# Kernel tuning notes

Measured on AMD Instinct MI355X. Metric: run time of the kernel, lower is better.

The kernel has to match this reference:

```python
import jax, jax.numpy as jnp
import numpy as np

NN_SIZE = 16  # nn_size from __init__


def _knn_idx(points_ref, k):
    """Brute-force KNN of points_ref against itself (replaces faiss_knn).
    Returns (B, N, k) neighbor indices, self point excluded."""
    sq = jnp.sum(points_ref * points_ref, axis=-1)  # (B, N)
    # squared pairwise distances (B, N, N)
    d2 = sq[:, :, None] + sq[:, None, :] - 2.0 * jnp.einsum(
        'bnd,bmd->bnm', points_ref, points_ref)
    _, idx = jax.lax.top_k(-d2, k + 1)  # nearest first; idx[...,0] is self
    return idx[:, :, 1:]


def _edge_lengths(pts, knn_idx):
    """Gather neighbor coords and compute edge lengths (B, N, K)."""
    group = jax.vmap(lambda p, i: p[i])(pts, knn_idx)  # (B, N, K, D)
    return jnp.linalg.norm(group - pts[:, :, None, :], axis=-1)


def setup_inputs() -> dict:
    key = jax.random.key(0)
    k1, k2 = jax.random.split(key)
    B, N, D = 4, 8192, 3
    points_ref = jax.random.normal(k1, (B, N, D), dtype=jnp.float32)
    # pred points: perturbed ref so the loss is non-degenerate
    points = points_ref + 0.01 * jax.random.normal(k2, (B, N, D), dtype=jnp.float32)
    return {"points_ref": points_ref, "points": points}


def reference(points_ref, points):
    # faiss KNN is non-differentiable -> stop_gradient on the index search
    knn_idx = _knn_idx(jax.lax.stop_gradient(points_ref), NN_SIZE)  # (B,N,K)
    dist_ref = _edge_lengths(points_ref, knn_idx)  # (B, N, K)
    dist = _edge_lengths(points, knn_idx)          # (B, N, K)
    # metric = torch.nn.L1Loss() (mean reduction)
    return jnp.mean(jnp.abs(dist_ref - dist))
```

## Files before the change

### kernel.cpp

```cpp
#include <hip/hip_runtime.h>
#include <math.h>

#define BATCH 4
#define NPTS  8192
#define KNN   16
#define KK    17
#define NQ    (BATCH*NPTS)
#define JMASK 0x1FFFu
#define EMASK 0xFFFFE000u
#define TOTAL_EDGES (BATCH*NPTS*KNN)

#define GC    32
#define GLO   (-4.5f)
#define GINV  (32.0f/9.0f)
#define NCELL (GC*GC*GC)

#define NG    128
#define GSZ   64

#define QPB   16
#define BLOCK 256
#define GRIDQ (NQ/QPB)
#define WIN   64
#define CAP   21

__device__ __forceinline__ int cell_coord(float x) {
    int c = (int)floorf((x - GLO) * GINV);
    return min(GC - 1, max(0, c));
}
__device__ __forceinline__ unsigned spread5(unsigned v) {
    v &= 31u;
    v = (v | (v << 8)) & 0x100Fu;
    v = (v | (v << 4)) & 0x10C3u;
    v = (v | (v << 2)) & 0x1249u;
    return v;
}
__device__ __forceinline__ unsigned morton_id(float x, float y, float z) {
    return spread5((unsigned)cell_coord(x)) | (spread5((unsigned)cell_coord(y)) << 1)
         | (spread5((unsigned)cell_coord(z)) << 2);
}
__device__ __forceinline__ unsigned mkkey(const float4 p, float xi, float yi,
                                          float zi, float sqi, unsigned j) {
    const float e  = fmaf(p.x, xi, fmaf(p.y, yi, p.z * zi)) + p.w;
    const float d2 = e + sqi;
    return (__float_as_uint(d2) & EMASK) | j;
}
__device__ __forceinline__ void ins17(unsigned (&a)[KK], unsigned key) {
    #pragma unroll
    for (int k = KK - 1; k >= 1; --k) a[k] = min(a[k], max(a[k - 1], key));
    a[0] = min(a[0], key);
}
template<int RL>
__device__ __forceinline__ unsigned merge_tau(const unsigned (*s_key)[BLOCK], int t) {
    const int mq = t & (QPB - 1), half = (t >> 4) & 1;
    unsigned m[KK];
    #pragma unroll
    for (int k = 0; k < KK; ++k) m[k] = 0xFFFFFFFFu;
    for (int s = 8 * half; s < 8 * half + 8; ++s) {
        const int col = mq + s * QPB;
        for (int k = 0; k < RL; ++k) {
            const unsigned c = s_key[k][col];
            if (c >= m[KK - 1]) break;
            ins17(m, c);
        }
    }
    unsigned tau = 0;
    #pragma unroll
    for (int k = 0; k < KK; ++k) {
        const unsigned bk = (unsigned)__shfl_xor((int)m[KK - 1 - k], 16, 64);
        tau = max(tau, min(m[k], bk));
    }
    return tau;
}

__global__ void pel_hist(const float* __restrict__ pref, unsigned* __restrict__ hist,
                         float* __restrict__ acc, unsigned* __restrict__ bcnt) {
    const int idx = blockIdx.x * 256 + threadIdx.x;
    if (idx == 0) { acc[0] = 0.0f; bcnt[0] = 0u; }
    const int b = idx >> 13;
    const unsigned mid = morton_id(pref[3*idx], pref[3*idx+1], pref[3*idx+2]);
    atomicAdd(&hist[b * NCELL + mid], 1u);
}
__global__ __launch_bounds__(1024)
void pel_scan(const unsigned* __restrict__ hist, unsigned* __restrict__ off) {
    __shared__ unsigned s[1024];
    const unsigned* h = hist + blockIdx.x * NCELL;
    unsigned*       o = off  + blockIdx.x * NCELL;
    const int t = threadIdx.x;
    unsigned v[32], tot = 0;
    #pragma unroll
    for (int k = 0; k < 32; ++k) { v[k] = h[t * 32 + k]; tot += v[k]; }
    s[t] = tot;
    __syncthreads();
    for (int d = 1; d < 1024; d <<= 1) {
        const unsigned add = (t >= d) ? s[t - d] : 0u;
        __syncthreads();
        s[t] += add;
        __syncthreads();
    }
    unsigned run = s[t] - tot;
    #pragma unroll
    for (int k = 0; k < 32; ++k) { o[t * 32 + k] = run; run += v[k]; }
}
__global__ void pel_scatter(const float* __restrict__ pref, const float* __restrict__ pts,
                            unsigned* __restrict__ off,
                            float4* __restrict__ p4r, float4* __restrict__ p4p) {
    const int idx = blockIdx.x * 256 + threadIdx.x;
    const int b = idx >> 13;
    const float x = pref[3*idx], y = pref[3*idx+1], z = pref[3*idx+2];
    const unsigned mid = morton_id(x, y, z);
    const unsigned pos = atomicAdd(&off[b * NCELL + mid], 1u);
    p4r[b * NPTS + pos] = make_float4(-2.f*x, -2.f*y, -2.f*z, fmaf(x, x, fmaf(y, y, z*z)));
    const float px = pts[3*idx], py = pts[3*idx+1], pz = pts[3*idx+2];
    p4p[b * NPTS + pos] = make_float4(-2.f*px, -2.f*py, -2.f*pz,
                                      fmaf(px, px, fmaf(py, py, pz*pz)));
}
__global__ __launch_bounds__(256)
void pel_gstat(const float4* __restrict__ P4r, float4* __restrict__ gball) {
    const int wv = threadIdx.x >> 6, lane = threadIdx.x & 63;
    const int gid = blockIdx.x * 4 + wv;
    const int b = gid >> 7, g = gid & (NG - 1);
    const float4 p = P4r[b * NPTS + g * GSZ + lane];
    const float x = -0.5f * p.x, y = -0.5f * p.y, z = -0.5f * p.z;
    float mnx = x, mxx = x, mny = y, mxy = y, mnz = z, mxz = z;
    #pragma unroll
    for (int m = 1; m <= 32; m <<= 1) {
        mnx = fminf(mnx, __shfl_xor(mnx, m, 64)); mxx = fmaxf(mxx, __shfl_xor(mxx, m, 64));
        mny = fminf(mny, __shfl_xor(mny, m, 64)); mxy = fmaxf(mxy, __shfl_xor(mxy, m, 64));
        mnz = fminf(mnz, __shfl_xor(mnz, m, 64)); mxz = fmaxf(mxz, __shfl_xor(mxz, m, 64));
    }
    const float cx = 0.5f * (mnx + mxx), cy = 0.5f * (mny + mxy), cz = 0.5f * (mnz + mxz);
    float d = sqrtf((x-cx)*(x-cx) + (y-cy)*(y-cy) + (z-cz)*(z-cz));
    #pragma unroll
    for (int m = 1; m <= 32; m <<= 1) d = fmaxf(d, __shfl_xor(d, m, 64));
    if (lane == 0) gball[gid] = make_float4(cx, cy, cz, d);
}

__global__ __launch_bounds__(BLOCK, 8)
void pel_query(const float4* __restrict__ P4r, const float4* __restrict__ P4p,
               const float4* __restrict__ gball,
               float* __restrict__ acc_ws, unsigned* __restrict__ bcnt,
               float* __restrict__ out)
{
    __shared__ unsigned s_key[CAP][BLOCK];
    __shared__ unsigned s_tau[QPB];
    __shared__ unsigned short s_glist[NG];
    __shared__ float s_grp[4];
    __shared__ int s_ng;
    __shared__ float s_part[BLOCK / 64];

    const int t  = threadIdx.x;
    const int lq = t & (QPB - 1), sp = t >> 4;
    const int q  = blockIdx.x * QPB + lq;
    const int b  = q >> 13;
    const int i  = q & (NPTS - 1);

    const float4* __restrict__ Pq = P4r + b * NPTS;
    const float4* __restrict__ Pp = P4p + b * NPTS;
    const float4* __restrict__ Gb = gball + b * NG;

    const float4 self = Pq[i];
    const float xi = -0.5f * self.x, yi = -0.5f * self.y, zi = -0.5f * self.z;
    const float sqi = self.w;

    unsigned al[4] = {~0u, ~0u, ~0u, ~0u};
    const int w0 = min(max(i - WIN / 2, 0), NPTS - WIN) + sp * 4;
    {
        float4 cw[4];
        #pragma unroll
        for (int u = 0; u < 4; ++u) cw[u] = Pq[w0 + u];
        #pragma unroll
        for (int u = 0; u < 4; ++u) {
            const unsigned key = mkkey(cw[u], xi, yi, zi, sqi, (unsigned)(w0 + u));
            #pragma unroll
            for (int k = 3; k >= 1; --k) al[k] = min(al[k], max(al[k - 1], key));
            al[0] = min(al[0], key);
        }
    }
    #pragma unroll
    for (int k = 0; k < 4; ++k) s_key[k][t] = al[k];
    __syncthreads();
    if (t < 32) {
        const unsigned tau0 = merge_tau<4>(s_key, t);
        if (t < QPB) s_tau[t] = tau0;
    }
    __syncthreads();

    if (t < QPB) {
        if (t == 0) s_ng = 0;
        const int i2 = (blockIdx.x * QPB + t) & (NPTS - 1);
        const float4 s2 = Pq[i2];
        const float qx = -0.5f * s2.x, qy = -0.5f * s2.y, qz = -0.5f * s2.z;
        float mnx = qx, mxx = qx, mny = qy, mxy = qy, mnz = qz, mxz = qz;
        #pragma unroll
        for (int m = 1; m <= 8; m <<= 1) {
            mnx = fminf(mnx, __shfl_xor(mnx, m, 64)); mxx = fmaxf(mxx, __shfl_xor(mxx, m, 64));
            mny = fminf(mny, __shfl_xor(mny, m, 64)); mxy = fmaxf(mxy, __shfl_xor(mxy, m, 64));
            mnz = fminf(mnz, __shfl_xor(mnz, m, 64)); mxz = fmaxf(mxz, __shfl_xor(mxz, m, 64));
        }
        const float cx = 0.5f * (mnx + mxx), cy = 0.5f * (mny + mxy), cz = 0.5f * (mnz + mxz);
        const float dq = sqrtf((qx-cx)*(qx-cx) + (qy-cy)*(qy-cy) + (qz-cz)*(qz-cz));
        const float rt = sqrtf(__uint_as_float((s_tau[t] & EMASK) + 0x2000u));
        float v = dq + rt;
        #pragma unroll
        for (int m = 1; m <= 8; m <<= 1) v = fmaxf(v, __shfl_xor(v, m, 64));
        if (t == 0) {
            s_grp[0] = cx; s_grp[1] = cy; s_grp[2] = cz; s_grp[3] = v + 1e-3f;
        }
    }
    __syncthreads();

    if (t < NG) {
        const float4 gb = Gb[t];
        const float dx = gb.x - s_grp[0], dy = gb.y - s_grp[1], dz = gb.z - s_grp[2];
        const float rhs = s_grp[3] + gb.w;
        if (dx*dx + dy*dy + dz*dz <= rhs * rhs) {
            const int slot = atomicAdd(&s_ng, 1);
            s_glist[slot] = (unsigned short)t;
        }
    }
    __syncthreads();
    const int ng = s_ng;

    unsigned tauL = s_tau[lq];
    int cnt = 0;
    for (int gi = 0; gi < ng; ++gi) {
        const int gb4 = (int)s_glist[gi] * GSZ + sp * 4;
        float4 c[4];
        #pragma unroll
        for (int u = 0; u < 4; ++u) c[u] = Pq[gb4 + u];
        #pragma unroll
        for (int u = 0; u < 4; ++u) {
            const unsigned key = mkkey(c[u], xi, yi, zi, sqi, (unsigned)(gb4 + u));
            s_key[cnt][t] = key;
            cnt += (key <= tauL) ? 1 : 0;
        }
        if (cnt > CAP - 4) {
            unsigned k17[KK];
            #pragma unroll
            for (int k = 0; k < KK; ++k) k17[k] = 0xFFFFFFFFu;
            for (int n = 0; n < cnt; ++n) ins17(k17, s_key[n][t]);
            const unsigned th = k17[KK - 1];
            int kept = 0;
            for (int n = 0; n < cnt; ++n) {
                const unsigned c2 = s_key[n][t];
                if (c2 <= th) { s_key[kept][t] = c2; ++kept; }
            }
            cnt = kept; tauL = min(tauL, th);
        }
    }

    unsigned c17[KK];
    #pragma unroll
    for (int k = 0; k < KK; ++k) c17[k] = 0xFFFFFFFFu;
    for (int n = 0; n < cnt; ++n) ins17(c17, s_key[n][t]);
    __syncthreads();
    #pragma unroll
    for (int k = 0; k < KK; ++k) s_key[k][t] = c17[k];
    __syncthreads();
    if (t < 32) {
        const unsigned tauX = merge_tau<KK>(s_key, t);
        if (t < QPB) s_tau[t] = tauX;
    }
    __syncthreads();
    const unsigned tauK = s_tau[lq];

    const float4 selfp = Pp[i];
    const float pxi = -0.5f * selfp.x, pyi = -0.5f * selfp.y, pzi = -0.5f * selfp.z;
    float accv = 0.0f;
    #pragma unroll
    for (int k = 0; k < KK; ++k) {
        if (c17[k] <= tauK) {
            const int j = (int)(c17[k] & JMASK);
            const float4 pr = Pq[j];
            const float er  = fmaf(pr.x, xi, fmaf(pr.y, yi, pr.z * zi)) + pr.w;
            const float d2r = fmaxf(er + sqi, 0.0f);
            const float4 pp = Pp[j];
            const float ep  = fmaf(pp.x, pxi, fmaf(pp.y, pyi, pp.z * pzi)) + pp.w;
            const float d2p = fmaxf(ep + selfp.w, 0.0f);
            accv += fabsf(sqrtf(d2r) - sqrtf(d2p));
        }
    }

    #pragma unroll
    for (int o = 32; o > 0; o >>= 1) accv += __shfl_down(accv, o, 64);
    if ((t & 63) == 0) s_part[t >> 6] = accv;
    __syncthreads();
    if (t == 0) {
        float s = 0.0f;
        #pragma unroll
        for (int w2 = 0; w2 < BLOCK / 64; ++w2) s += s_part[w2];
        atomicAdd(acc_ws, s);
        __threadfence();
        const unsigned old = atomicAdd(bcnt, 1u);
        if (old == GRIDQ - 1) {
            __threadfence();
            const float total = atomicAdd(acc_ws, 0.0f);
            out[0] = total * (1.0f / (float)TOTAL_EDGES);
        }
    }
}

extern "C" void kernel_launch(void* const* d_in, const int* in_sizes, int n_in,
                              void* d_out, int out_size, void* d_ws, size_t ws_size,
                              hipStream_t stream) {
    const float* pref = (const float*)d_in[0];
    const float* pts  = (const float*)d_in[1];
    float4*   P4r  = (float4*)d_ws;
    float4*   P4p  = P4r + NQ;
    unsigned* hist = (unsigned*)d_ws;
    unsigned* off  = (unsigned*)((char*)d_ws + 1048576);
    float4*   gball= (float4*)((char*)d_ws + 1572864);
    float*    acc  = (float*)((char*)d_ws + 1581056);
    unsigned* bcnt = (unsigned*)(acc + 1);
    float*    out  = (float*)d_out;

    hipMemsetAsync(hist, 0, BATCH * NCELL * sizeof(unsigned), stream);
    pel_hist   <<<NQ / 256, 256, 0, stream>>>(pref, hist, acc, bcnt);
    pel_scan   <<<BATCH, 1024, 0, stream>>>(hist, off);
    pel_scatter<<<NQ / 256, 256, 0, stream>>>(pref, pts, off, P4r, P4p);
    pel_gstat  <<<(BATCH * NG) / 4, 256, 0, stream>>>(P4r, gball);
    pel_query  <<<GRIDQ, BLOCK, 0, stream>>>(P4r, P4p, gball, acc, bcnt, out);
}
```

Baseline: 254.9 us.

## Stage candidate groups in shared memory tiles and swizzle block order

Candidate points from up to 16 selected groups are now loaded cooperatively by the whole block into an LDS tile. Every thread then reads them from shared memory instead of issuing per-thread global float4 loads for each group. Block IDs are remapped so that consecutive blocks spread across query groups, and launch bounds drop from 8 to 4 blocks per CU to make room for the extra LDS. The cost is added __syncthreads per tile, more LDS use and possibly lower occupancy.

```diff
diff --git a/kernel.cpp b/kernel.cpp
--- a/kernel.cpp
+++ b/kernel.cpp
@@ -23,6 +23,7 @@
 #define GRIDQ (NQ/QPB)
 #define WIN   64
 #define CAP   21
+#define SG    16
 
 __device__ __forceinline__ int cell_coord(float x) {
     int c = (int)floorf((x - GLO) * GINV);
@@ -136,13 +137,15 @@
     if (lane == 0) gball[gid] = make_float4(cx, cy, cz, d);
 }
 
-__global__ __launch_bounds__(BLOCK, 8)
+__global__ __launch_bounds__(BLOCK, 4)
 void pel_query(const float4* __restrict__ P4r, const float4* __restrict__ P4p,
                const float4* __restrict__ gball,
                float* __restrict__ acc_ws, unsigned* __restrict__ bcnt,
                float* __restrict__ out)
 {
     __shared__ unsigned s_key[CAP][BLOCK];
+    __shared__ float4 s_cand[SG * GSZ];
+    __shared__ unsigned s_gbase[SG];
     __shared__ unsigned s_tau[QPB];
     __shared__ unsigned short s_glist[NG];
     __shared__ float s_grp[4];
@@ -151,7 +154,9 @@
 
     const int t  = threadIdx.x;
     const int lq = t & (QPB - 1), sp = t >> 4;
-    const int q  = blockIdx.x * QPB + lq;
+    const int bid = blockIdx.x;
+    const int qg  = ((bid & 7) << 8) | (bid >> 3);
+    const int q  = qg * QPB + lq;
     const int b  = q >> 13;
     const int i  = q & (NPTS - 1);
 
@@ -188,7 +193,7 @@
 
     if (t < QPB) {
         if (t == 0) s_ng = 0;
-        const int i2 = (blockIdx.x * QPB + t) & (NPTS - 1);
+        const int i2 = (qg * QPB + t) & (NPTS - 1);
         const float4 s2 = Pq[i2];
         const float qx = -0.5f * s2.x, qy = -0.5f * s2.y, qz = -0.5f * s2.z;
         float mnx = qx, mxx = qx, mny = qy, mxy = qy, mnz = qz, mxz = qz;
@@ -224,29 +229,48 @@
 
     unsigned tauL = s_tau[lq];
     int cnt = 0;
-    for (int gi = 0; gi < ng; ++gi) {
-        const int gb4 = (int)s_glist[gi] * GSZ + sp * 4;
-        float4 c[4];
-        #pragma unroll
-        for (int u = 0; u < 4; ++u) c[u] = Pq[gb4 + u];
-        #pragma unroll
-        for (int u = 0; u < 4; ++u) {
-            const unsigned key = mkkey(c[u], xi, yi, zi, sqi, (unsigned)(gb4 + u));
-            s_key[cnt][t] = key;
-            cnt += (key <= tauL) ? 1 : 0;
-        }
-        if (cnt > CAP - 4) {
-            unsigned k17[KK];
+    for (int tile = 0; tile < ng; tile += SG) {
+        const int tng = min(SG, ng - tile);
+        __syncthreads();
+        if (t < tng) s_gbase[t] = (unsigned)s_glist[tile + t] * GSZ;
+        {
+            unsigned srcs[4]; int mm[4]; int nm = 0;
+            for (int m = t; m < tng * GSZ; m += BLOCK) {
+                mm[nm] = m;
+                srcs[nm] = (unsigned)s_glist[tile + (m >> 6)] * GSZ + (m & 63);
+                ++nm;
+            }
+            float4 vals[4];
+            for (int k = 0; k < nm; ++k) vals[k] = Pq[srcs[k]];
+            for (int k = 0; k < nm; ++k) s_cand[mm[k]] = vals[k];
+        }
+        __syncthreads();
+        const int nsteps = tng * 4;
+        for (int mblk = 0; mblk < nsteps; mblk += 4) {
+            const unsigned jbase = s_gbase[mblk >> 2];
+            float4 c[4];
             #pragma unroll
-            for (int k = 0; k < KK; ++k) k17[k] = 0xFFFFFFFFu;
-            for (int n = 0; n < cnt; ++n) ins17(k17, s_key[n][t]);
-            const unsigned th = k17[KK - 1];
-            int kept = 0;
-            for (int n = 0; n < cnt; ++n) {
-                const unsigned c2 = s_key[n][t];
-                if (c2 <= th) { s_key[kept][t] = c2; ++kept; }
+            for (int u = 0; u < 4; ++u) c[u] = s_cand[(mblk + u) * 16 + sp];
+            #pragma unroll
+            for (int u = 0; u < 4; ++u) {
+                const unsigned j = jbase + (unsigned)(((mblk + u) * 16 + sp) & 63);
+                const unsigned key = mkkey(c[u], xi, yi, zi, sqi, j);
+                s_key[cnt][t] = key;
+                cnt += (key <= tauL) ? 1 : 0;
             }
-            cnt = kept; tauL = min(tauL, th);
+            if (cnt > CAP - 4) {
+                unsigned k17[KK];
+                #pragma unroll
+                for (int k = 0; k < KK; ++k) k17[k] = 0xFFFFFFFFu;
+                for (int n = 0; n < cnt; ++n) ins17(k17, s_key[n][t]);
+                const unsigned th = k17[KK - 1];
+                int kept = 0;
+                for (int n = 0; n < cnt; ++n) {
+                    const unsigned c2 = s_key[n][t];
+                    if (c2 <= th) { s_key[kept][t] = c2; ++kept; }
+                }
+                cnt = kept; tauL = min(tauL, th);
+            }
         }
     }
 
```

After: 351.5 us. 1.38x slower.

## Scan a contiguous group range, coarsen the Morton grid, and swizzle query blocks

Applied to the files above, without the earlier changes.

The query kernel now keeps only the minimum and maximum index of the overlapping point groups and scans that whole contiguous range, rather than building an explicit list of overlapping groups. Each thread takes a contiguous chunk of the range instead of 4 points per group. The Morton grid is coarsened from 32^3 to 16^3 cells, which shrinks the histogram and prefix-scan work, and block indices are swizzled to reorder queries across the grid. The range scan drops the shared-memory list but may visit many groups that do not overlap, and the coarser grid gives a looser spatial sort.

```diff
diff --git a/kernel.cpp b/kernel.cpp
--- a/kernel.cpp
+++ b/kernel.cpp
@@ -10,9 +10,9 @@
 #define EMASK 0xFFFFE000u
 #define TOTAL_EDGES (BATCH*NPTS*KNN)
 
-#define GC    32
+#define GC    16
 #define GLO   (-4.5f)
-#define GINV  (32.0f/9.0f)
+#define GINV  (16.0f/9.0f)
 #define NCELL (GC*GC*GC)
 
 #define NG    128
@@ -28,16 +28,15 @@
     int c = (int)floorf((x - GLO) * GINV);
     return min(GC - 1, max(0, c));
 }
-__device__ __forceinline__ unsigned spread5(unsigned v) {
-    v &= 31u;
-    v = (v | (v << 8)) & 0x100Fu;
-    v = (v | (v << 4)) & 0x10C3u;
-    v = (v | (v << 2)) & 0x1249u;
+__device__ __forceinline__ unsigned spread4(unsigned v) {
+    v &= 15u;
+    v = (v | (v << 4)) & 0xC3u;
+    v = (v | (v << 2)) & 0x249u;
     return v;
 }
 __device__ __forceinline__ unsigned morton_id(float x, float y, float z) {
-    return spread5((unsigned)cell_coord(x)) | (spread5((unsigned)cell_coord(y)) << 1)
-         | (spread5((unsigned)cell_coord(z)) << 2);
+    return spread4((unsigned)cell_coord(x)) | (spread4((unsigned)cell_coord(y)) << 1)
+         | (spread4((unsigned)cell_coord(z)) << 2);
 }
 __device__ __forceinline__ unsigned mkkey(const float4 p, float xi, float yi,
                                           float zi, float sqi, unsigned j) {
@@ -87,9 +86,9 @@
     const unsigned* h = hist + blockIdx.x * NCELL;
     unsigned*       o = off  + blockIdx.x * NCELL;
     const int t = threadIdx.x;
-    unsigned v[32], tot = 0;
-    #pragma unroll
-    for (int k = 0; k < 32; ++k) { v[k] = h[t * 32 + k]; tot += v[k]; }
+    unsigned v[4], tot = 0;
+    #pragma unroll
+    for (int k = 0; k < 4; ++k) { v[k] = h[t * 4 + k]; tot += v[k]; }
     s[t] = tot;
     __syncthreads();
     for (int d = 1; d < 1024; d <<= 1) {
@@ -100,7 +99,7 @@
     }
     unsigned run = s[t] - tot;
     #pragma unroll
-    for (int k = 0; k < 32; ++k) { o[t * 32 + k] = run; run += v[k]; }
+    for (int k = 0; k < 4; ++k) { o[t * 4 + k] = run; run += v[k]; }
 }
 __global__ void pel_scatter(const float* __restrict__ pref, const float* __restrict__ pts,
                             unsigned* __restrict__ off,
@@ -144,14 +143,15 @@
 {
     __shared__ unsigned s_key[CAP][BLOCK];
     __shared__ unsigned s_tau[QPB];
-    __shared__ unsigned short s_glist[NG];
     __shared__ float s_grp[4];
-    __shared__ int s_ng;
+    __shared__ int s_glo, s_ghi;
     __shared__ float s_part[BLOCK / 64];
 
     const int t  = threadIdx.x;
     const int lq = t & (QPB - 1), sp = t >> 4;
-    const int q  = blockIdx.x * QPB + lq;
+    const int bid = blockIdx.x;
+    const int qg  = ((bid & 7) << 8) | (bid >> 3);
+    const int q  = qg * QPB + lq;
     const int b  = q >> 13;
     const int i  = q & (NPTS - 1);
 
@@ -187,8 +187,8 @@
     __syncthreads();
 
     if (t < QPB) {
-        if (t == 0) s_ng = 0;
-        const int i2 = (blockIdx.x * QPB + t) & (NPTS - 1);
+        if (t == 0) { s_glo = NG; s_ghi = 0; }
+        const int i2 = (qg * QPB + t) & (NPTS - 1);
         const float4 s2 = Pq[i2];
         const float qx = -0.5f * s2.x, qy = -0.5f * s2.y, qz = -0.5f * s2.z;
         float mnx = qx, mxx = qx, mny = qy, mxy = qy, mnz = qz, mxz = qz;
@@ -215,23 +215,24 @@
         const float dx = gb.x - s_grp[0], dy = gb.y - s_grp[1], dz = gb.z - s_grp[2];
         const float rhs = s_grp[3] + gb.w;
         if (dx*dx + dy*dy + dz*dz <= rhs * rhs) {
-            const int slot = atomicAdd(&s_ng, 1);
-            s_glist[slot] = (unsigned short)t;
-        }
-    }
-    __syncthreads();
-    const int ng = s_ng;
+            atomicMin(&s_glo, t);
+            atomicMax(&s_ghi, t);
+        }
+    }
+    __syncthreads();
+    const int glo = s_glo, ghi = s_ghi;
 
     unsigned tauL = s_tau[lq];
     int cnt = 0;
-    for (int gi = 0; gi < ng; ++gi) {
-        const int gb4 = (int)s_glist[gi] * GSZ + sp * 4;
+    const int csz = (ghi - glo + 1) * 4;
+    const int c0  = glo * GSZ + sp * csz;
+    for (int j = c0; j < c0 + csz; j += 4) {
         float4 c[4];
         #pragma unroll
-        for (int u = 0; u < 4; ++u) c[u] = Pq[gb4 + u];
+        for (int u = 0; u < 4; ++u) c[u] = Pq[j + u];
         #pragma unroll
         for (int u = 0; u < 4; ++u) {
-            const unsigned key = mkkey(c[u], xi, yi, zi, sqi, (unsigned)(gb4 + u));
+            const unsigned key = mkkey(c[u], xi, yi, zi, sqi, (unsigned)(j + u));
             s_key[cnt][t] = key;
             cnt += (key <= tauL) ? 1 : 0;
         }
@@ -310,8 +311,8 @@
     float4*   P4p  = P4r + NQ;
     unsigned* hist = (unsigned*)d_ws;
     unsigned* off  = (unsigned*)((char*)d_ws + 1048576);
-    float4*   gball= (float4*)((char*)d_ws + 1572864);
-    float*    acc  = (float*)((char*)d_ws + 1581056);
+    float4*   gball= (float4*)((char*)d_ws + 1114112);
+    float*    acc  = (float*)((char*)d_ws + 1122304);
     unsigned* bcnt = (unsigned*)(acc + 1);
     float*    out  = (float*)d_out;
 
```

New measurement: 670.6 us. 2.63x slower.
